# Performance work log

Hardware: AMD Instinct MI355X
Metric: run time of the kernel (lower is better)

Reference implementation:

```python
import jax, jax.numpy as jnp
import numpy as np

HIDDEN = 768
HEADS = 12
HEAD_DIM = HIDDEN // HEADS

def setup_inputs() -> dict:
    key = jax.random.key(0)
    ks = jax.random.split(key, 9)
    s = 1.0 / np.sqrt(HIDDEN)
    x = jax.random.normal(ks[0], (2, 2048, HIDDEN), dtype=jnp.float32)
    Wq = jax.random.normal(ks[1], (HIDDEN, HIDDEN), dtype=jnp.float32) * s
    bq = jnp.zeros((HIDDEN,), dtype=jnp.float32)
    Wk = jax.random.normal(ks[2], (HIDDEN, HIDDEN), dtype=jnp.float32) * s
    bk = jnp.zeros((HIDDEN,), dtype=jnp.float32)
    Wv = jax.random.normal(ks[3], (HIDDEN, HIDDEN), dtype=jnp.float32) * s
    bv = jnp.zeros((HIDDEN,), dtype=jnp.float32)
    Wo = jax.random.normal(ks[4], (HIDDEN, HIDDEN), dtype=jnp.float32) * s
    bo = jnp.zeros((HIDDEN,), dtype=jnp.float32)
    return {"x": x, "Wq": Wq, "bq": bq, "Wk": Wk, "bk": bk,
            "Wv": Wv, "bv": bv, "Wo": Wo, "bo": bo}

def reference(x, Wq, bq, Wk, bk, Wv, bv, Wo, bo):
    B, S, _ = x.shape
    # project and split heads: [B, H, S, D]
    def proj(W, b):
        return (x @ W + b).reshape(B, S, HEADS, HEAD_DIM).transpose(0, 2, 1, 3)
    q = proj(Wq, bq)
    k = proj(Wk, bk)
    v = proj(Wv, bv)
    # NOTE: original module does NOT scale by 1/sqrt(head_dim)
    scores = jnp.einsum('bhqd,bhkd->bhqk', q, k)
    attn = jax.nn.softmax(scores, axis=-1)
    out = jnp.einsum('bhqk,bhkd->bhqd', attn, v)
    out = out.transpose(0, 2, 1, 3).reshape(B, S, HIDDEN)
    return out @ Wo + bo
```

## Files before the change

### kernel.cpp

```cpp
#include <hip/hip_runtime.h>
#include <cstddef>

#define HIDDEN 768
#define NHEADS 12
#define HDIM   64
#define BATCH  2
#define SEQ    2048
#define NROWS  (BATCH*SEQ)
#define LOG2E  1.4426950408889634f

typedef float f32x4  __attribute__((ext_vector_type(4)));
typedef float f32x16 __attribute__((ext_vector_type(16)));
typedef short bf16x8 __attribute__((ext_vector_type(8)));

__device__ __forceinline__ float fast_exp2(float x){
    return __builtin_amdgcn_exp2f(x);
}

__device__ __forceinline__ unsigned short f2bf(float f){
    unsigned u = __builtin_bit_cast(unsigned, f);
    u = u + 0x7FFFu + ((u >> 16) & 1u);
    return (unsigned short)(u >> 16);
}
__device__ __forceinline__ unsigned packbf2(float a, float b){
    unsigned ua = (__builtin_bit_cast(unsigned, a) + 0x8000u) >> 16;
    unsigned ub = (__builtin_bit_cast(unsigned, b) + 0x8000u) & 0xFFFF0000u;
    return ua | ub;
}
__device__ __forceinline__ unsigned cvtpk_bf16(float a, float b){
    unsigned r;
    asm("v_cvt_pk_bf16_f32 %0, %1, %2" : "=v"(r) : "v"(a), "v"(b));
    return r;
}

__device__ __forceinline__ void gl_lds16(const unsigned short* g, unsigned short* l){
    __builtin_amdgcn_global_load_lds(
        (const __attribute__((address_space(1))) unsigned int*)g,
        (__attribute__((address_space(3))) unsigned int*)l, 16, 0, 0);
}

__global__ __launch_bounds__(256) void cvt_bf16(const float* __restrict__ in,
                                                unsigned short* __restrict__ out,
                                                int n4)
{
    const int i = blockIdx.x * 256 + threadIdx.x;
    if (i >= n4) return;
    const float4 v = reinterpret_cast<const float4*>(in)[i];
    ushort4 o;
    o.x = f2bf(v.x); o.y = f2bf(v.y); o.z = f2bf(v.z); o.w = f2bf(v.w);
    reinterpret_cast<ushort4*>(out)[i] = o;
}

__global__ __launch_bounds__(256) void transpose_cvt4(const float* __restrict__ W0,
                                                      const float* __restrict__ W1,
                                                      const float* __restrict__ W2,
                                                      const float* __restrict__ W3,
                                                      unsigned short* __restrict__ T0,
                                                      unsigned short* __restrict__ T1,
                                                      unsigned short* __restrict__ T2,
                                                      unsigned short* __restrict__ T3)
{
    const int z = blockIdx.z;
    const float* W = (z == 0) ? W0 : (z == 1) ? W1 : (z == 2) ? W2 : W3;
    unsigned short* Wt = (z == 0) ? T0 : (z == 1) ? T1 : (z == 2) ? T2 : T3;

    __shared__ unsigned short t[64][66];
    const int k0 = blockIdx.y * 64, n0 = blockIdx.x * 64;
    const int row = threadIdx.x >> 2;
    const int c0  = (threadIdx.x & 3) * 16;
#pragma unroll
    for (int j = 0; j < 16; j += 4) {
        const float4 v = *reinterpret_cast<const float4*>(&W[(size_t)(k0 + row) * HIDDEN + n0 + c0 + j]);
        t[row][c0 + j + 0] = f2bf(v.x);
        t[row][c0 + j + 1] = f2bf(v.y);
        t[row][c0 + j + 2] = f2bf(v.z);
        t[row][c0 + j + 3] = f2bf(v.w);
    }
    __syncthreads();
#pragma unroll
    for (int j = 0; j < 16; j += 4) {
        ushort4 o;
        o.x = t[c0 + j + 0][row];
        o.y = t[c0 + j + 1][row];
        o.z = t[c0 + j + 2][row];
        o.w = t[c0 + j + 3][row];
        *reinterpret_cast<ushort4*>(&Wt[(size_t)(n0 + row) * HIDDEN + k0 + c0 + j]) = o;
    }
}

__device__ __forceinline__ void gemm_body(const unsigned short* __restrict__ A,
                                          const unsigned short* __restrict__ Wt,
                                          const float* __restrict__ bias,
                                          void* __restrict__ Cout, int mode,
                                          float scale,
                                          unsigned short* As, unsigned short* Bs)
{
    const int tid = threadIdx.x;
    const int l = tid & 63, w = tid >> 6;
    const int wm = w >> 1, wn = w & 1;
    const int l15 = l & 15, lg = l >> 4;
    const int srow = l >> 3, sslot = l & 7;
    const int m0 = blockIdx.y * 64, n0 = blockIdx.x * 96;

    f32x4 acc[2][3] = {};

    for (int k0 = 0; k0 < HIDDEN; k0 += 64) {
        __syncthreads();
#pragma unroll
        for (int a = 0; a < 2; ++a) {
            const int row = (a * 4 + w) * 8 + srow;
            const int sl = sslot ^ (row & 7);
            gl_lds16(&A[(size_t)(m0 + row) * HIDDEN + k0 + sl * 8], &As[(a * 4 + w) * 512]);
        }
#pragma unroll
        for (int b = 0; b < 3; ++b) {
            const int row = (b * 4 + w) * 8 + srow;
            const int sl = sslot ^ (row & 7);
            gl_lds16(&Wt[(size_t)(n0 + row) * HIDDEN + k0 + sl * 8], &Bs[(b * 4 + w) * 512]);
        }
        __syncthreads();

#pragma unroll
        for (int kk = 0; kk < 2; ++kk) {
            bf16x8 af[2], bfr[3];
#pragma unroll
            for (int mi = 0; mi < 2; ++mi) {
                const int r = wm * 32 + mi * 16 + l15;
                af[mi] = *reinterpret_cast<const bf16x8*>(&As[r * 64 + ((lg * 8 + kk * 32) ^ ((r & 7) << 3))]);
            }
#pragma unroll
            for (int ni = 0; ni < 3; ++ni) {
                const int r = wn * 48 + ni * 16 + l15;
                bfr[ni] = *reinterpret_cast<const bf16x8*>(&Bs[r * 64 + ((lg * 8 + kk * 32) ^ ((r & 7) << 3))]);
            }
#pragma unroll
            for (int mi = 0; mi < 2; ++mi)
#pragma unroll
                for (int ni = 0; ni < 3; ++ni)
                    acc[mi][ni] = __builtin_amdgcn_mfma_f32_16x16x32_bf16(af[mi], bfr[ni], acc[mi][ni], 0, 0, 0);
        }
    }

#pragma unroll
    for (int mi = 0; mi < 2; ++mi) {
#pragma unroll
        for (int ni = 0; ni < 3; ++ni) {
#pragma unroll
            for (int rr = 0; rr < 4; ++rr) {
                const int row = m0 + wm * 32 + mi * 16 + lg * 4 + rr;
                const int col = n0 + wn * 48 + ni * 16 + l15;
                const float v = (acc[mi][ni][rr] + bias[col]) * scale;
                if (mode == 0) {
                    const int b = row >> 11, s = row & (SEQ - 1);
                    const int hh = col >> 6, d = col & (HDIM - 1);
                    ((unsigned short*)Cout)[(((size_t)b * NHEADS + hh) * SEQ + s) * HDIM + d] = f2bf(v);
                } else if (mode == 1) {
                    const int b = row >> 11, s = row & (SEQ - 1);
                    const int hh = col >> 6, d = col & (HDIM - 1);
                    ((unsigned short*)Cout)[(((size_t)b * NHEADS + hh) * HDIM + d) * SEQ + s] = f2bf(v);
                } else {
                    ((float*)Cout)[(size_t)row * HIDDEN + col] = v;
                }
            }
        }
    }
}

__global__ __launch_bounds__(256) void qkv_gemm(const unsigned short* __restrict__ A,
                                                const unsigned short* __restrict__ Wqt,
                                                const unsigned short* __restrict__ Wkt,
                                                const unsigned short* __restrict__ Wvt,
                                                const float* __restrict__ bq,
                                                const float* __restrict__ bk,
                                                const float* __restrict__ bv,
                                                unsigned short* __restrict__ Qb,
                                                unsigned short* __restrict__ Kb,
                                                unsigned short* __restrict__ Vtb)
{
    __shared__ unsigned short As[64 * 64];
    __shared__ unsigned short Bs[96 * 64];
    const int z = blockIdx.z;
    const unsigned short* Wt = (z == 0) ? Wqt : (z == 1) ? Wkt : Wvt;
    const float* bias = (z == 0) ? bq : (z == 1) ? bk : bv;
    void* out = (z == 0) ? (void*)Qb : (z == 1) ? (void*)Kb : (void*)Vtb;
    const int mode = (z == 2) ? 1 : 0;
    const float scale = (z == 0) ? LOG2E : 1.0f;
    gemm_body(A, Wt, bias, out, mode, scale, As, Bs);
}

__global__ __launch_bounds__(256) void out_gemm(const unsigned short* __restrict__ A,
                                                const unsigned short* __restrict__ Wt,
                                                const float* __restrict__ bias,
                                                float* __restrict__ Cout)
{
    __shared__ unsigned short As[64 * 64];
    __shared__ unsigned short Bs[96 * 64];
    gemm_body(A, Wt, bias, Cout, 2, 1.0f, As, Bs);
}

__global__ __launch_bounds__(256) void attn_mfma(const unsigned short* __restrict__ Q,
                                                 const unsigned short* __restrict__ K,
                                                 const unsigned short* __restrict__ Vt,
                                                 unsigned short* __restrict__ O)
{
    __shared__ __align__(16) char shraw[33792];
    unsigned short* Ks  = (unsigned short*)shraw;
    unsigned short* Vs  = (unsigned short*)(shraw + 16384);
    float*          xch = (float*)shraw;
    unsigned int*   Ep  = (unsigned int*)(shraw + 16384);
    float2*         mlx = (float2*)(shraw + 32768);

    const int tid = threadIdx.x;
    const int l = tid & 63;
    const int wq2 = (tid >> 6) & 1;
    const int wkv = tid >> 7;
    const int l31 = l & 31, hi = l >> 5;
    const int lr = l >> 3, slot = l & 7;
    const int q0 = blockIdx.x * 64;
    const int h = blockIdx.y, b = blockIdx.z;
    const size_t base = ((size_t)b * NHEADS + h) * (size_t)SEQ * HDIM;

    const int q = q0 + wq2 * 32 + l31;
    bf16x8 qf[4];
#pragma unroll
    for (int t = 0; t < 4; ++t)
        qf[t] = *reinterpret_cast<const bf16x8*>(&Q[base + (size_t)q * HDIM + 16 * t + 8 * hi]);

    f32x16 accO[2] = {};
    float m = -1e30f, lsum = 0.f;

    unsigned short* Kb = Ks + wkv * 4096;
    unsigned short* Vb = Vs + wkv * 4096;
    const int kvbase = wkv * (SEQ / 2);

    for (int i = 0; i < SEQ / 128; ++i) {
        const int t0 = kvbase + i * 64;
        __syncthreads();
#pragma unroll
        for (int j = 0; j < 4; ++j) {
            const int row = (j * 2 + wq2) * 8 + lr;
            const int sl = slot ^ (row & 7);
            gl_lds16(&K [base + (size_t)(t0 + row) * HDIM + sl * 8], &Kb[(j * 2 + wq2) * 512]);
            gl_lds16(&Vt[base + (size_t)row * SEQ + t0 + sl * 8],    &Vb[(j * 2 + wq2) * 512]);
        }
        __syncthreads();

        f32x16 s0v = {}, s1v = {};
        __builtin_amdgcn_s_setprio(1);
#pragma unroll
        for (int t = 0; t < 4; ++t) {
            const int co = 16 * t + 8 * hi;
            const int r0 = l31, r1 = 32 + l31;
            const bf16x8 k0 = *reinterpret_cast<const bf16x8*>(&Kb[r0 * 64 + (co ^ ((r0 & 7) << 3))]);
            const bf16x8 k1 = *reinterpret_cast<const bf16x8*>(&Kb[r1 * 64 + (co ^ ((r1 & 7) << 3))]);
            s0v = __builtin_amdgcn_mfma_f32_32x32x16_bf16(k0, qf[t], s0v, 0, 0, 0);
            s1v = __builtin_amdgcn_mfma_f32_32x32x16_bf16(k1, qf[t], s1v, 0, 0, 0);
        }
        __builtin_amdgcn_s_setprio(0);

        float tmax = -1e30f;
#pragma unroll
        for (int r = 0; r < 16; r += 4) {
            tmax = fmaxf(tmax, fmaxf(fmaxf(s0v[r], s0v[r + 1]), fmaxf(s0v[r + 2], s0v[r + 3])));
            tmax = fmaxf(tmax, fmaxf(fmaxf(s1v[r], s1v[r + 1]), fmaxf(s1v[r + 2], s1v[r + 3])));
        }
        tmax = fmaxf(tmax, __shfl_xor(tmax, 32));

        if (tmax > m + 8.f) {
            const float scl = fast_exp2(m - tmax);
            lsum *= scl;
#pragma unroll
            for (int r = 0; r < 16; ++r) { accO[0][r] *= scl; accO[1][r] *= scl; }
            m = tmax;
        }

        unsigned wv[16];
        float ls = 0.f;
#pragma unroll
        for (int a = 0; a < 8; ++a) {
            const float pa = fast_exp2(s0v[2 * a] - m);
            const float pb = fast_exp2(s0v[2 * a + 1] - m);
            ls += pa + pb;
            wv[a] = cvtpk_bf16(pa, pb);
        }
#pragma unroll
        for (int a = 0; a < 8; ++a) {
            const float pa = fast_exp2(s1v[2 * a] - m);
            const float pb = fast_exp2(s1v[2 * a + 1] - m);
            ls += pa + pb;
            wv[8 + a] = cvtpk_bf16(pa, pb);
        }
        ls += __shfl_xor(ls, 32);
        lsum += ls;

#pragma unroll
        for (int slot2 = 0; slot2 < 4; ++slot2) {
            unsigned a0 = wv[slot2 * 4 + 0], a2 = wv[slot2 * 4 + 2];
            unsigned a1 = wv[slot2 * 4 + 1], a3 = wv[slot2 * 4 + 3];
            asm volatile("v_permlane32_swap_b32 %0, %1" : "+v"(a0), "+v"(a2));
            asm volatile("v_permlane32_swap_b32 %0, %1" : "+v"(a1), "+v"(a3));
            uint4 fr;
            fr.x = a0;
            fr.y = a1;
            fr.z = a2;
            fr.w = a3;
            const bf16x8 pfrag = __builtin_bit_cast(bf16x8, fr);
            __builtin_amdgcn_s_setprio(1);
#pragma unroll
            for (int db = 0; db < 2; ++db) {
                const int vr = 32 * db + l31;
                const int co = (16 * slot2 + 8 * hi) ^ ((vr & 7) << 3);
                const bf16x8 vf = *reinterpret_cast<const bf16x8*>(&Vb[vr * 64 + co]);
                accO[db] = __builtin_amdgcn_mfma_f32_32x32x16_bf16(vf, pfrag, accO[db], 0, 0, 0);
            }
            __builtin_amdgcn_s_setprio(0);
        }
    }

    __syncthreads();
    if (!hi) mlx[(wq2 * 2 + wkv) * 32 + l31] = make_float2(m, lsum);
    __syncthreads();
    const float2 mp = mlx[(wq2 * 2 + (1 - wkv)) * 32 + l31];
    const float M  = fmaxf(m, mp.x);
    const float s  = fast_exp2(m - M);
    const float lf = lsum * s + mp.y * fast_exp2(mp.x - M);

    if (wkv == 1) {
#pragma unroll
        for (int db = 0; db < 2; ++db)
#pragma unroll
            for (int r = 0; r < 16; ++r) {
                const int d = 32 * db + (r & 3) + 8 * (r >> 2) + 4 * hi;
                xch[wq2 * 2048 + d * 32 + l31] = accO[db][r] * s;
            }
    }
    __syncthreads();
    if (wkv == 0) {
        const float inv = 1.f / lf;
#pragma unroll
        for (int db = 0; db < 2; ++db)
#pragma unroll
            for (int r = 0; r < 16; ++r) {
                const int d = 32 * db + (r & 3) + 8 * (r >> 2) + 4 * hi;
                accO[db][r] = (accO[db][r] * s + xch[wq2 * 2048 + d * 32 + l31]) * inv;
            }
#pragma unroll
        for (int db = 0; db < 2; ++db)
#pragma unroll
            for (int a = 0; a < 8; ++a) {
                const unsigned wd = packbf2(accO[db][2 * a], accO[db][2 * a + 1]);
                const int pi = 16 * db + 4 * (a >> 1) + (a & 1) + 2 * hi;
                Ep[(wq2 * 32 + l31) * 33 + pi] = wd;
            }
    }
    __syncthreads();
    if (wkv == 0) {
#pragma unroll
        for (int pss = 0; pss < 4; ++pss) {
            const int idx = pss * 64 + l;
            const int qr = idx >> 3, c = idx & 7;
            uint4 ov;
            ov.x = Ep[(wq2 * 32 + qr) * 33 + c * 4 + 0];
            ov.y = Ep[(wq2 * 32 + qr) * 33 + c * 4 + 1];
            ov.z = Ep[(wq2 * 32 + qr) * 33 + c * 4 + 2];
            ov.w = Ep[(wq2 * 32 + qr) * 33 + c * 4 + 3];
            *reinterpret_cast<uint4*>(&O[((size_t)b * SEQ + q0 + wq2 * 32 + qr) * HIDDEN + h * HDIM + c * 8]) = ov;
        }
    }
}

extern "C" void kernel_launch(void* const* d_in, const int* in_sizes, int n_in,
                              void* d_out, int out_size, void* d_ws, size_t ws_size,
                              hipStream_t stream)
{
    const float* x  = (const float*)d_in[0];
    const float* Wq = (const float*)d_in[1];
    const float* bq = (const float*)d_in[2];
    const float* Wk = (const float*)d_in[3];
    const float* bk = (const float*)d_in[4];
    const float* Wv = (const float*)d_in[5];
    const float* bv = (const float*)d_in[6];
    const float* Wo = (const float*)d_in[7];
    const float* bo = (const float*)d_in[8];
    float* out = (float*)d_out;

    unsigned short* p = (unsigned short*)d_ws;
    const size_t szX = (size_t)NROWS * HIDDEN;
    const size_t szW = (size_t)HIDDEN * HIDDEN;
    const size_t szH = (size_t)BATCH * NHEADS * SEQ * HDIM;
    unsigned short* xb  = p;              p += szX;
    unsigned short* Wqt = p;              p += szW;
    unsigned short* Wkt = p;              p += szW;
    unsigned short* Wvt = p;              p += szW;
    unsigned short* Wot = p;              p += szW;
    unsigned short* Qb  = p;              p += szH;
    unsigned short* Kb  = p;              p += szH;
    unsigned short* Vtb = p;              p += szH;
    unsigned short* Oab = p;              p += szX;

    cvt_bf16<<<(int)(szX / 4 + 255) / 256, 256, 0, stream>>>(x, xb, (int)(szX / 4));
    transpose_cvt4<<<dim3(HIDDEN / 64, HIDDEN / 64, 4), 256, 0, stream>>>(
        Wq, Wk, Wv, Wo, Wqt, Wkt, Wvt, Wot);

    qkv_gemm<<<dim3(HIDDEN / 96, NROWS / 64, 3), 256, 0, stream>>>(
        xb, Wqt, Wkt, Wvt, bq, bk, bv, Qb, Kb, Vtb);

    attn_mfma<<<dim3(SEQ / 64, NHEADS, BATCH), 256, 0, stream>>>(Qb, Kb, Vtb, Oab);

    out_gemm<<<dim3(HIDDEN / 96, NROWS / 64), 256, 0, stream>>>(Oab, Wot, bo, out);
}
```

Measured before the change: 109.8 us.

## Double-buffer LDS tiles in projection GEMMs to overlap loads with MFMA

The QKV and output projection GEMMs now use two LDS buffers. The next K-slice is issued into one buffer while MFMAs consume the other, and the k-loop is fully unrolled into six ping-pong iterations. This hides global-to-LDS latency behind compute and drops one barrier per slice. In exchange, LDS per block doubles (to 40 KB), which may reduce occupancy. Correctness depends on whether gl_lds16 completes before the barrier.

```diff
diff --git a/kernel.cpp b/kernel.cpp
--- a/kernel.cpp
+++ b/kernel.cpp
@@ -88,6 +88,47 @@
     }
 }
 
+#define G_STAGE(buf, k0) do {                                                                  \
+    unsigned short* Ad = As + (buf) * 4096;                                                    \
+    unsigned short* Bd = Bs + (buf) * 6144;                                                    \
+    _Pragma("unroll")                                                                          \
+    for (int a_ = 0; a_ < 2; ++a_) {                                                           \
+        const int row_ = (a_ * 4 + w) * 8 + srow;                                              \
+        const int sl_ = sslot ^ (row_ & 7);                                                    \
+        gl_lds16(&A[(size_t)(m0 + row_) * HIDDEN + (k0) + sl_ * 8], &Ad[(a_ * 4 + w) * 512]);  \
+    }                                                                                          \
+    _Pragma("unroll")                                                                          \
+    for (int b_ = 0; b_ < 3; ++b_) {                                                           \
+        const int row_ = (b_ * 4 + w) * 8 + srow;                                              \
+        const int sl_ = sslot ^ (row_ & 7);                                                    \
+        gl_lds16(&Wt[(size_t)(n0 + row_) * HIDDEN + (k0) + sl_ * 8], &Bd[(b_ * 4 + w) * 512]); \
+    }                                                                                          \
+} while (0)
+
+#define G_COMPUTE(buf) do {                                                                    \
+    unsigned short* Ad = As + (buf) * 4096;                                                    \
+    unsigned short* Bd = Bs + (buf) * 6144;                                                    \
+    _Pragma("unroll")                                                                          \
+    for (int kk = 0; kk < 2; ++kk) {                                                           \
+        bf16x8 af[2], bfr[3];                                                                  \
+        _Pragma("unroll")                                                                      \
+        for (int mi = 0; mi < 2; ++mi) {                                                       \
+            const int r_ = wm * 32 + mi * 16 + l15;                                            \
+            af[mi] = *reinterpret_cast<const bf16x8*>(&Ad[r_ * 64 + ((lg * 8 + kk * 32) ^ ((r_ & 7) << 3))]); \
+        }                                                                                      \
+        _Pragma("unroll")                                                                      \
+        for (int ni = 0; ni < 3; ++ni) {                                                       \
+            const int r_ = wn * 48 + ni * 16 + l15;                                            \
+            bfr[ni] = *reinterpret_cast<const bf16x8*>(&Bd[r_ * 64 + ((lg * 8 + kk * 32) ^ ((r_ & 7) << 3))]); \
+        }                                                                                      \
+        _Pragma("unroll")                                                                      \
+        for (int mi = 0; mi < 2; ++mi)                                                         \
+            _Pragma("unroll")                                                                  \
+            for (int ni = 0; ni < 3; ++ni)                                                     \
+                acc[mi][ni] = __builtin_amdgcn_mfma_f32_16x16x32_bf16(af[mi], bfr[ni], acc[mi][ni], 0, 0, 0); \
+    }                                                                                          \
+} while (0)
+
 __device__ __forceinline__ void gemm_body(const unsigned short* __restrict__ A,
                                           const unsigned short* __restrict__ Wt,
                                           const float* __restrict__ bias,
@@ -104,41 +145,16 @@
 
     f32x4 acc[2][3] = {};
 
-    for (int k0 = 0; k0 < HIDDEN; k0 += 64) {
+    G_STAGE(0, 0);
+    __syncthreads();
+#pragma unroll
+    for (int i = 0; i < 6; ++i) {
+        G_STAGE(1, (2 * i + 1) * 64);
+        G_COMPUTE(0);
         __syncthreads();
-#pragma unroll
-        for (int a = 0; a < 2; ++a) {
-            const int row = (a * 4 + w) * 8 + srow;
-            const int sl = sslot ^ (row & 7);
-            gl_lds16(&A[(size_t)(m0 + row) * HIDDEN + k0 + sl * 8], &As[(a * 4 + w) * 512]);
-        }
-#pragma unroll
-        for (int b = 0; b < 3; ++b) {
-            const int row = (b * 4 + w) * 8 + srow;
-            const int sl = sslot ^ (row & 7);
-            gl_lds16(&Wt[(size_t)(n0 + row) * HIDDEN + k0 + sl * 8], &Bs[(b * 4 + w) * 512]);
-        }
+        if (i < 5) G_STAGE(0, (2 * i + 2) * 64);
+        G_COMPUTE(1);
         __syncthreads();
-
-#pragma unroll
-        for (int kk = 0; kk < 2; ++kk) {
-            bf16x8 af[2], bfr[3];
-#pragma unroll
-            for (int mi = 0; mi < 2; ++mi) {
-                const int r = wm * 32 + mi * 16 + l15;
-                af[mi] = *reinterpret_cast<const bf16x8*>(&As[r * 64 + ((lg * 8 + kk * 32) ^ ((r & 7) << 3))]);
-            }
-#pragma unroll
-            for (int ni = 0; ni < 3; ++ni) {
-                const int r = wn * 48 + ni * 16 + l15;
-                bfr[ni] = *reinterpret_cast<const bf16x8*>(&Bs[r * 64 + ((lg * 8 + kk * 32) ^ ((r & 7) << 3))]);
-            }
-#pragma unroll
-            for (int mi = 0; mi < 2; ++mi)
-#pragma unroll
-                for (int ni = 0; ni < 3; ++ni)
-                    acc[mi][ni] = __builtin_amdgcn_mfma_f32_16x16x32_bf16(af[mi], bfr[ni], acc[mi][ni], 0, 0, 0);
-        }
     }
 
 #pragma unroll
@@ -177,8 +193,8 @@
                                                 unsigned short* __restrict__ Kb,
                                                 unsigned short* __restrict__ Vtb)
 {
-    __shared__ unsigned short As[64 * 64];
-    __shared__ unsigned short Bs[96 * 64];
+    __shared__ unsigned short As[2 * 4096];
+    __shared__ unsigned short Bs[2 * 6144];
     const int z = blockIdx.z;
     const unsigned short* Wt = (z == 0) ? Wqt : (z == 1) ? Wkt : Wvt;
     const float* bias = (z == 0) ? bq : (z == 1) ? bk : bv;
@@ -193,8 +209,8 @@
                                                 const float* __restrict__ bias,
                                                 float* __restrict__ Cout)
 {
-    __shared__ unsigned short As[64 * 64];
-    __shared__ unsigned short Bs[96 * 64];
+    __shared__ unsigned short As[2 * 4096];
+    __shared__ unsigned short Bs[2 * 6144];
     gemm_body(A, Wt, bias, Cout, 2, 1.0f, As, Bs);
 }
 
```

After: 118.3 us. 7.7% more time.
